# Optimization experiments

Hardware: AMD Instinct MI355X
Metric: run time of the kernel (lower is better)

## Reference

```python
import jax, jax.numpy as jnp
import numpy as np

N_ENT = 50000
N_REL = 237
DIM = 200
BATCH = 1024
N_EDGE_RAW = 400000
WALK_LEN = 3


def _build_graph():
    rng = np.random.default_rng(0)
    src = rng.integers(0, N_ENT, N_EDGE_RAW)
    dst = rng.integers(0, N_ENT, N_EDGE_RAW)
    key = np.unique(src.astype(np.int64) * N_ENT + dst.astype(np.int64))
    row = (key // N_ENT).astype(np.int64)
    col = (key % N_ENT).astype(np.int64)
    # symmetric D^{-1/2} A D^{-1/2} normalization (binary coalesced adjacency)
    deg = np.bincount(row, minlength=N_ENT).astype(np.float64)
    dinv = np.where(deg > 0, deg ** -0.5, 0.0)
    adj_val = (dinv[row] * dinv[col]).astype(np.float32)
    # random walk of length 3 from every node (torch_cluster.random_walk semantics)
    rowptr = np.concatenate([[0], np.cumsum(np.bincount(row, minlength=N_ENT))]).astype(np.int64)
    cur = np.arange(N_ENT)
    walk = [cur]
    for _ in range(WALK_LEN):
        d = rowptr[cur + 1] - rowptr[cur]
        off = np.floor(rng.random(N_ENT) * np.maximum(d, 1)).astype(np.int64)
        idx = np.minimum(rowptr[cur] + off, len(row) - 1)
        nxt = np.where(d > 0, col[idx], cur)
        walk.append(nxt)
        cur = nxt
    walk = np.stack(walk, 1)  # (N, WALK_LEN+1)
    # scatter(rw_adj, 1, walk, 1): binary rows, duplicates collapse; then D^{-1} row-normalize
    rw_key = np.unique(np.repeat(np.arange(N_ENT), WALK_LEN + 1).astype(np.int64) * N_ENT + walk.reshape(-1))
    rw_row = (rw_key // N_ENT).astype(np.int64)
    rw_col = (rw_key % N_ENT).astype(np.int64)
    rw_deg = np.bincount(rw_row, minlength=N_ENT).astype(np.float64)
    rw_val = (1.0 / np.maximum(rw_deg[rw_row], 1.0)).astype(np.float32)
    return row, col, adj_val, rw_row, rw_col, rw_val


def setup_inputs() -> dict:
    row, col, adj_val, rw_row, rw_col, rw_val = _build_graph()
    E = row.shape[0]
    key = jax.random.key(0)
    ks = jax.random.split(key, 12)
    g = 0.05
    return dict(
        entity_emb=jax.random.normal(ks[0], (N_ENT, DIM), jnp.float32) * g,
        rel_emb=jax.random.normal(ks[1], (2 * N_REL, DIM * DIM), jnp.float32) * 0.01,
        node_W1=jax.random.normal(ks[2], (2, DIM, DIM), jnp.float32) * g,
        node_b1=jnp.zeros((2, DIM), jnp.float32),
        node_W2=jax.random.normal(ks[3], (2, DIM, 1), jnp.float32) * g,
        node_b2=jnp.zeros((2, 1), jnp.float32),
        edge_W1=jax.random.normal(ks[4], (2, 2 * DIM, DIM), jnp.float32) * g,
        edge_b1=jnp.zeros((2, DIM), jnp.float32),
        edge_W2=jax.random.normal(ks[5], (2, DIM, 1), jnp.float32) * g,
        edge_b2=jnp.zeros((2, 1), jnp.float32),
        adj_row=jnp.asarray(row), adj_col=jnp.asarray(col), adj_val=jnp.asarray(adj_val),
        rw_row=jnp.asarray(rw_row), rw_col=jnp.asarray(rw_col), rw_val=jnp.asarray(rw_val),
        node_eps=jax.random.uniform(ks[6], (2, N_ENT, 1), jnp.float32),
        edge_eps=jax.random.uniform(ks[7], (2, E, 1), jnp.float32),
        sub=jax.random.randint(ks[8], (BATCH,), 0, N_ENT),
        rel=jax.random.randint(ks[9], (BATCH,), 0, 2 * N_REL),
        obj=jax.random.randint(ks[10], (BATCH,), 0, N_ENT),
        neg_tail=jax.random.randint(ks[11], (BATCH, 2), 0, N_ENT),
    )


def _spmm(row, col, val, x, n):
    # sparse COO (row, col, val) @ dense x, output (n, d)
    return jax.ops.segment_sum(val[:, None] * x[col], row, num_segments=n)


def _gate(logits, u):
    # concrete-gate noise: eps ~ U(bias, 1-bias); sigmoid((logit(eps)+logits)/0.5)
    bias = 1e-4
    eps = (2.0 * bias - 1.0) * u + (1.0 - bias)
    return jax.nn.sigmoid((jnp.log(eps) - jnp.log1p(-eps) + logits) / 0.5)


def reference(entity_emb, rel_emb, node_W1, node_b1, node_W2, node_b2,
              edge_W1, edge_b1, edge_W2, edge_b2,
              adj_row, adj_col, adj_val, rw_row, rw_col, rw_val,
              node_eps, edge_eps, sub, rel, obj, neg_tail):
    n, d = entity_emb.shape
    e0 = entity_emb
    node_masks, edge_masks = [], []
    edge_cat = jnp.concatenate([e0[adj_row], e0[adj_col]], axis=-1)  # (E, 2d)
    for i in range(2):
        h = jax.nn.relu(e0 @ node_W1[i] + node_b1[i])
        node_masks.append(_gate(h @ node_W2[i] + node_b2[i], node_eps[i]))  # (n,1)
        he = jax.nn.relu(edge_cat @ edge_W1[i] + edge_b1[i])
        edge_masks.append(_gate(he @ edge_W2[i] + edge_b2[i], edge_eps[i])[:, 0])  # (E,)
    # node-drop branch: mix self vs random-walk mean-pooled, then GCN propagate
    x_nd = e0
    for i in range(2):
        mp = _spmm(rw_row, rw_col, rw_val, x_nd, n)
        x_nd = node_masks[i] * x_nd + (1.0 - node_masks[i]) * mp
        x_nd = _spmm(adj_row, adj_col, adj_val, x_nd, n)
    # edge-drop branch: rw propagation twice; only the LAST edge mask is applied (as in source)
    x_ed = e0
    new_edge = adj_val
    for i in range(2):
        x_ed = _spmm(rw_row, rw_col, rw_val, x_ed, n)
        new_edge = adj_val * edge_masks[i]
    x_ed = _spmm(adj_row, adj_col, new_edge, x_ed, n)
    # RESCAL scoring against all entities
    lhs1 = e0[sub]                                   # (B, d)
    rel1 = rel_emb[rel].reshape(-1, d, d)            # (B, d, d)
    self_hr = jnp.einsum('bd,bde->be', lhs1, rel1)   # (B, d)
    scores = jax.nn.sigmoid(self_hr @ e0.T)          # (B, n)
    return scores, x_nd, x_ed
```

## Files before the change

### kernel.cpp

```cpp
#include <hip/hip_runtime.h>
#include <math.h>

#define DIMV 200
typedef unsigned short ushort;
typedef unsigned int uint;
typedef __attribute__((ext_vector_type(8))) __bf16  bf16x8;
typedef __attribute__((ext_vector_type(4))) float   f32x4;

static __device__ __forceinline__ int lower_bound(const int* __restrict__ a, int n, int key) {
    int lo = 0, hi = n;
    while (lo < hi) {
        int mid = (lo + hi) >> 1;
        if (a[mid] < key) lo = mid + 1; else hi = mid;
    }
    return lo;
}

static __device__ __forceinline__ float gate_fn(float u, float logit) {
    float ee = fmaf(u, -0.9998f, 0.9999f);
    float g  = (logf(ee) - log1pf(-ee) + logit) * 2.0f;
    return 1.0f / (1.0f + expf(-g));
}

static __device__ __forceinline__ ushort f2bf(float f) {
    unsigned int u = __float_as_uint(f);
    return (ushort)((u + 0x7fffu + ((u >> 16) & 1u)) >> 16);
}
static __device__ __forceinline__ float2 bfp2f(uint u) {
    float2 r;
    r.x = __uint_as_float(u << 16);
    r.y = __uint_as_float(u & 0xffff0000u);
    return r;
}
static __device__ __forceinline__ uint f2bfp(float a, float b) {
    return (uint)f2bf(a) | ((uint)f2bf(b) << 16);
}

static __device__ __forceinline__ void cvt8_store(ushort* dst, const float* src) {
    float4 a = *(const float4*)src;
    float4 b = *(const float4*)(src + 4);
    dst[0] = f2bf(a.x); dst[1] = f2bf(a.y); dst[2] = f2bf(a.z); dst[3] = f2bf(a.w);
    dst[4] = f2bf(b.x); dst[5] = f2bf(b.y); dst[6] = f2bf(b.z); dst[7] = f2bf(b.w);
}
static __device__ __forceinline__ void zero8_store(ushort* dst) {
#pragma unroll
    for (int i = 0; i < 8; i++) dst[i] = 0;
}

__global__ __launch_bounds__(256) void prep_all(
    const float* __restrict__ e0, ushort* __restrict__ e0bf,
    const float* __restrict__ w1e_src, ushort* __restrict__ W1eT,
    const float* __restrict__ w1n_src, ushort* __restrict__ W1nT,
    const int* __restrict__ adj_row, int E, int* __restrict__ rp_adj,
    const int* __restrict__ rw_row, int Erw, int* __restrict__ rp_rw,
    const float* __restrict__ rel_emb, const int* __restrict__ sub,
    const int* __restrict__ rel, ushort* __restrict__ hrbf, int N)
{
    __shared__ float lhs[DIMV];
    int bid = blockIdx.x;
    const int t = threadIdx.x;

    const int NB0 = (N * 28 + 255) >> 8;
    if (bid < NB0) {
        int idx = bid * 256 + t;
        if (idx < N * 28) {
            int n = idx / 28, c = idx % 28;
            ushort* dst = e0bf + (size_t)n * 224 + c * 8;
            if (c < 25) cvt8_store(dst, e0 + (size_t)n * 200 + c * 8);
            else        zero8_store(dst);
        }
        return;
    }
    bid -= NB0;
    if (bid < 364) {
        int idx = bid * 256 + t;
        if (idx < 416 * 224) {
            int n = idx / 224, k = idx % 224;
            float v = 0.f;
            if (k < 200) {
                if (n < 200)      v = w1e_src[k * 200 + n];
                else if (n < 400) v = w1e_src[(k + 200) * 200 + (n - 200)];
            }
            W1eT[idx] = f2bf(v);
        }
        return;
    }
    bid -= 364;
    if (bid < 364) {
        int i = bid / 182;
        int idx = (bid % 182) * 256 + t;
        if (idx < 208 * 224) {
            int n = idx / 224, k = idx % 224;
            float v = (n < 200 && k < 200) ? w1n_src[i * 40000 + k * 200 + n] : 0.f;
            W1nT[(size_t)i * 208 * 224 + idx] = f2bf(v);
        }
        return;
    }
    bid -= 364;
    const int NBr = (N + 256) >> 8;
    if (bid < NBr) {
        int r = bid * 256 + t;
        if (r <= N) rp_adj[r] = lower_bound(adj_row, E, r);
        return;
    }
    bid -= NBr;
    if (bid < NBr) {
        int r = bid * 256 + t;
        if (r <= N) rp_rw[r] = lower_bound(rw_row, Erw, r);
        return;
    }
    bid -= NBr;
    {
        const int b = bid;
        if (t < DIMV) lhs[t] = e0[(size_t)sub[b] * DIMV + t];
        __syncthreads();
        if (t >= 224) return;
        if (t < DIMV) {
            const float* R = rel_emb + (size_t)rel[b] * (DIMV * DIMV);
            float acc = 0.f;
            for (int dd = 0; dd < DIMV; dd++)
                acc = fmaf(lhs[dd], R[dd * DIMV + t], acc);
            hrbf[(size_t)b * 224 + t] = f2bf(acc);
        } else {
            hrbf[(size_t)b * 224 + t] = 0;
        }
    }
}

__global__ __launch_bounds__(256) void fused_mlp(
    const ushort* __restrict__ e0bf, const ushort* __restrict__ W1eT,
    const ushort* __restrict__ W1nT, ushort* __restrict__ Pb,
    const float* __restrict__ nb1, const float* __restrict__ nW2,
    const float* __restrict__ nb2, const float* __restrict__ neps,
    float* __restrict__ node_mask, int N, int GX)
{
    __shared__ __align__(16) ushort As[2][128 * 40];
    __shared__ __align__(16) ushort Bs[2][208 * 40];
    __shared__ float bsh[208], wsh[208];

    const int r8  = blockIdx.x & 7;
    const int rem = blockIdx.x >> 3;
    const int y   = rem & 3;
    const int q4  = rem >> 2;
    const int x   = r8 + 8 * q4;
    if (x >= GX) return;

    const int t    = threadIdx.x;
    const int lane = t & 63;
    const int w    = t >> 6;
    const int q    = lane >> 4;
    const int ln   = lane & 15;
    const int r0   = x * 128;
    const bool edge = (y < 2);
    const int  i    = y - 2;
    const ushort* Wt = edge ? (W1eT + (size_t)y * 208 * 224)
                            : (W1nT + (size_t)i * 208 * 224);

    if (!edge && t < 208) {
        bsh[t] = (t < 200) ? nb1[i * 200 + t] : 0.f;
        wsh[t] = (t < 200) ? nW2[i * 200 + t] : 0.f;
    }

    f32x4 acc[2][13];
#pragma unroll
    for (int mt = 0; mt < 2; mt++)
#pragma unroll
        for (int nt = 0; nt < 13; nt++) {
            acc[mt][nt][0] = 0.f; acc[mt][nt][1] = 0.f;
            acc[mt][nt][2] = 0.f; acc[mt][nt][3] = 0.f;
        }

    auto stageA = [&](int ks, int buf) {
#pragma unroll
        for (int it = 0; it < 2; it++) {
            int f = t + it * 256;
            int m = f >> 2, c4 = f & 3;
            int g = r0 + m;
            ushort* dst = &As[buf][m * 40 + c4 * 8];
            if (g < N) *(bf16x8*)dst = *(const bf16x8*)&e0bf[(size_t)g * 224 + ks * 32 + c4 * 8];
            else       zero8_store(dst);
        }
    };
    auto stageB = [&](int ks, int buf) {
        for (int f = t; f < 832; f += 256) {
            int n = f >> 2, c4 = f & 3;
            *(bf16x8*)&Bs[buf][n * 40 + c4 * 8] =
                *(const bf16x8*)&Wt[(size_t)n * 224 + ks * 32 + c4 * 8];
        }
    };

    stageA(0, 0); stageB(0, 0);
    __syncthreads();

    for (int ks = 0; ks < 7; ks++) {
        int cur = ks & 1;
        if (ks + 1 < 7) { stageA(ks + 1, cur ^ 1); stageB(ks + 1, cur ^ 1); }
        bf16x8 af0 = *(const bf16x8*)&As[cur][(w * 32 + ln) * 40 + q * 8];
        bf16x8 af1 = *(const bf16x8*)&As[cur][(w * 32 + 16 + ln) * 40 + q * 8];
#pragma unroll
        for (int nt = 0; nt < 13; nt++) {
            bf16x8 bf = *(const bf16x8*)&Bs[cur][(nt * 16 + ln) * 40 + q * 8];
            acc[0][nt] = __builtin_amdgcn_mfma_f32_16x16x32_bf16(af0, bf, acc[0][nt], 0, 0, 0);
            acc[1][nt] = __builtin_amdgcn_mfma_f32_16x16x32_bf16(af1, bf, acc[1][nt], 0, 0, 0);
        }
        __syncthreads();
    }

    if (edge) {
#pragma unroll
        for (int mt = 0; mt < 2; mt++) {
            int gm = r0 + w * 32 + mt * 16 + q * 4;
#pragma unroll
            for (int nt = 0; nt < 13; nt++) {
                int gn = y * 208 + nt * 16 + ln;
                if (gn < 400) {
#pragma unroll
                    for (int r = 0; r < 4; r++)
                        if (gm + r < N) Pb[(size_t)(gm + r) * 400 + gn] = f2bf(acc[mt][nt][r]);
                }
            }
        }
    } else {
        float p[2][4];
#pragma unroll
        for (int mt = 0; mt < 2; mt++)
#pragma unroll
            for (int r = 0; r < 4; r++) {
                float s = 0.f;
#pragma unroll
                for (int nt = 0; nt < 13; nt++) {
                    int n = nt * 16 + ln;
                    float h = fmaxf(acc[mt][nt][r] + bsh[n], 0.f);
                    s = fmaf(h, wsh[n], s);
                }
                p[mt][r] = s;
            }
#pragma unroll
        for (int off = 1; off < 16; off <<= 1)
#pragma unroll
            for (int mt = 0; mt < 2; mt++)
#pragma unroll
                for (int r = 0; r < 4; r++)
                    p[mt][r] += __shfl_xor(p[mt][r], off);

        if (ln == 0) {
            float b2v = nb2[i];
            const float* epsi = neps + (size_t)i * N;
            float* outi = node_mask + (size_t)i * N;
#pragma unroll
            for (int mt = 0; mt < 2; mt++)
#pragma unroll
                for (int r = 0; r < 4; r++) {
                    int g = r0 + w * 32 + mt * 16 + q * 4 + r;
                    if (g < N) outi[g] = gate_fn(epsi[g], p[mt][r] + b2v);
                }
        }
    }
}

static __device__ __forceinline__ void spmm_bb_body(
    const uint* __restrict__ x, int xld, const int* __restrict__ rowptr,
    const int* __restrict__ col, const float* __restrict__ val,
    uint* __restrict__ out, int N, int vb, int t)
{
    const int w = t >> 6, lane = t & 63;
    const int r = vb * 4 + w;
    if (lane >= 50 || r >= N) return;
    const int off = 2 * lane;
    const int lo = rowptr[r], hi = rowptr[r + 1];
    float a0 = 0.f, a1 = 0.f, a2 = 0.f, a3 = 0.f;
    for (int e = lo; e < hi; e += 4) {
        int n = hi - e;
        int c0 = col[e];
        int c1 = n > 1 ? col[e + 1] : c0;
        int c2 = n > 2 ? col[e + 2] : c0;
        int c3 = n > 3 ? col[e + 3] : c0;
        float v0 = val[e];
        float v1 = n > 1 ? val[e + 1] : 0.f;
        float v2 = n > 2 ? val[e + 2] : 0.f;
        float v3 = n > 3 ? val[e + 3] : 0.f;
        uint2 u0 = *(const uint2*)&x[(size_t)c0 * xld + off];
        uint2 u1 = *(const uint2*)&x[(size_t)c1 * xld + off];
        uint2 u2 = *(const uint2*)&x[(size_t)c2 * xld + off];
        uint2 u3 = *(const uint2*)&x[(size_t)c3 * xld + off];
        float2 p;
        p = bfp2f(u0.x); a0 = fmaf(v0, p.x, a0); a1 = fmaf(v0, p.y, a1);
        p = bfp2f(u0.y); a2 = fmaf(v0, p.x, a2); a3 = fmaf(v0, p.y, a3);
        p = bfp2f(u1.x); a0 = fmaf(v1, p.x, a0); a1 = fmaf(v1, p.y, a1);
        p = bfp2f(u1.y); a2 = fmaf(v1, p.x, a2); a3 = fmaf(v1, p.y, a3);
        p = bfp2f(u2.x); a0 = fmaf(v2, p.x, a0); a1 = fmaf(v2, p.y, a1);
        p = bfp2f(u2.y); a2 = fmaf(v2, p.x, a2); a3 = fmaf(v2, p.y, a3);
        p = bfp2f(u3.x); a0 = fmaf(v3, p.x, a0); a1 = fmaf(v3, p.y, a1);
        p = bfp2f(u3.y); a2 = fmaf(v3, p.x, a2); a3 = fmaf(v3, p.y, a3);
    }
    *(uint2*)&out[(size_t)r * 100 + off] = make_uint2(f2bfp(a0, a1), f2bfp(a2, a3));
}

static __device__ __forceinline__ void dual_body(
    const uint* __restrict__ xA, const uint* __restrict__ xB,
    const int* __restrict__ rowptr, const int* __restrict__ col,
    const float* __restrict__ val, const float* __restrict__ emask,
    float* __restrict__ outA, uint* __restrict__ outB, int N, int vb, int t)
{
    const int w = t >> 6, lane = t & 63;
    const int r = vb * 4 + w;
    if (lane >= 50 || r >= N) return;
    const int off = 2 * lane;
    const int lo = rowptr[r], hi = rowptr[r + 1];
    float sA0=0.f,sA1=0.f,sA2=0.f,sA3=0.f;
    float sB0=0.f,sB1=0.f,sB2=0.f,sB3=0.f;
    for (int e = lo; e < hi; e += 4) {
        int n = hi - e;
        int c0 = col[e];
        int c1 = n > 1 ? col[e + 1] : c0;
        int c2 = n > 2 ? col[e + 2] : c0;
        int c3 = n > 3 ? col[e + 3] : c0;
        float v0 = val[e];
        float v1 = n > 1 ? val[e + 1] : 0.f;
        float v2 = n > 2 ? val[e + 2] : 0.f;
        float v3 = n > 3 ? val[e + 3] : 0.f;
        float m0 = v0 * emask[e];
        float m1 = n > 1 ? v1 * emask[e + 1] : 0.f;
        float m2 = n > 2 ? v2 * emask[e + 2] : 0.f;
        float m3 = n > 3 ? v3 * emask[e + 3] : 0.f;
        size_t o0 = (size_t)c0 * 100 + off, o1 = (size_t)c1 * 100 + off;
        size_t o2 = (size_t)c2 * 100 + off, o3 = (size_t)c3 * 100 + off;
        uint2 ua0 = *(const uint2*)&xA[o0], ua1 = *(const uint2*)&xA[o1];
        uint2 ua2 = *(const uint2*)&xA[o2], ua3 = *(const uint2*)&xA[o3];
        uint2 ub0 = *(const uint2*)&xB[o0], ub1 = *(const uint2*)&xB[o1];
        uint2 ub2 = *(const uint2*)&xB[o2], ub3 = *(const uint2*)&xB[o3];
        float2 p;
        p = bfp2f(ua0.x); sA0 = fmaf(m0, p.x, sA0); sA1 = fmaf(m0, p.y, sA1);
        p = bfp2f(ua0.y); sA2 = fmaf(m0, p.x, sA2); sA3 = fmaf(m0, p.y, sA3);
        p = bfp2f(ua1.x); sA0 = fmaf(m1, p.x, sA0); sA1 = fmaf(m1, p.y, sA1);
        p = bfp2f(ua1.y); sA2 = fmaf(m1, p.x, sA2); sA3 = fmaf(m1, p.y, sA3);
        p = bfp2f(ua2.x); sA0 = fmaf(m2, p.x, sA0); sA1 = fmaf(m2, p.y, sA1);
        p = bfp2f(ua2.y); sA2 = fmaf(m2, p.x, sA2); sA3 = fmaf(m2, p.y, sA3);
        p = bfp2f(ua3.x); sA0 = fmaf(m3, p.x, sA0); sA1 = fmaf(m3, p.y, sA1);
        p = bfp2f(ua3.y); sA2 = fmaf(m3, p.x, sA2); sA3 = fmaf(m3, p.y, sA3);
        p = bfp2f(ub0.x); sB0 = fmaf(v0, p.x, sB0); sB1 = fmaf(v0, p.y, sB1);
        p = bfp2f(ub0.y); sB2 = fmaf(v0, p.x, sB2); sB3 = fmaf(v0, p.y, sB3);
        p = bfp2f(ub1.x); sB0 = fmaf(v1, p.x, sB0); sB1 = fmaf(v1, p.y, sB1);
        p = bfp2f(ub1.y); sB2 = fmaf(v1, p.x, sB2); sB3 = fmaf(v1, p.y, sB3);
        p = bfp2f(ub2.x); sB0 = fmaf(v2, p.x, sB0); sB1 = fmaf(v2, p.y, sB1);
        p = bfp2f(ub2.y); sB2 = fmaf(v2, p.x, sB2); sB3 = fmaf(v2, p.y, sB3);
        p = bfp2f(ub3.x); sB0 = fmaf(v3, p.x, sB0); sB1 = fmaf(v3, p.y, sB1);
        p = bfp2f(ub3.y); sB2 = fmaf(v3, p.x, sB2); sB3 = fmaf(v3, p.y, sB3);
    }
    float4 oA; oA.x = sA0; oA.y = sA1; oA.z = sA2; oA.w = sA3;
    *(float4*)&outA[(size_t)r * 200 + 2 * off] = oA;
    *(uint2*)&outB[(size_t)r * 100 + off] = make_uint2(f2bfp(sB0, sB1), f2bfp(sB2, sB3));
}

static __device__ __forceinline__ void rwcomb_body(
    const uint* __restrict__ x, const int* __restrict__ rowptr,
    const int* __restrict__ col, const float* __restrict__ val,
    const float* __restrict__ mask, uint* __restrict__ out, int N, int vb, int t)
{
    const int w = t >> 6, lane = t & 63;
    const int r = vb * 4 + w;
    if (lane >= 50 || r >= N) return;
    const int off = 2 * lane;
    const int lo = rowptr[r], hi = rowptr[r + 1];
    float a0 = 0.f, a1 = 0.f, a2 = 0.f, a3 = 0.f;
    for (int e = lo; e < hi; e += 4) {
        int n = hi - e;
        int c0 = col[e];
        int c1 = n > 1 ? col[e + 1] : c0;
        int c2 = n > 2 ? col[e + 2] : c0;
        int c3 = n > 3 ? col[e + 3] : c0;
        float v0 = val[e];
        float v1 = n > 1 ? val[e + 1] : 0.f;
        float v2 = n > 2 ? val[e + 2] : 0.f;
        float v3 = n > 3 ? val[e + 3] : 0.f;
        uint2 u0 = *(const uint2*)&x[(size_t)c0 * 100 + off];
        uint2 u1 = *(const uint2*)&x[(size_t)c1 * 100 + off];
        uint2 u2 = *(const uint2*)&x[(size_t)c2 * 100 + off];
        uint2 u3 = *(const uint2*)&x[(size_t)c3 * 100 + off];
        float2 p;
        p = bfp2f(u0.x); a0 = fmaf(v0, p.x, a0); a1 = fmaf(v0, p.y, a1);
        p = bfp2f(u0.y); a2 = fmaf(v0, p.x, a2); a3 = fmaf(v0, p.y, a3);
        p = bfp2f(u1.x); a0 = fmaf(v1, p.x, a0); a1 = fmaf(v1, p.y, a1);
        p = bfp2f(u1.y); a2 = fmaf(v1, p.x, a2); a3 = fmaf(v1, p.y, a3);
        p = bfp2f(u2.x); a0 = fmaf(v2, p.x, a0); a1 = fmaf(v2, p.y, a1);
        p = bfp2f(u2.y); a2 = fmaf(v2, p.x, a2); a3 = fmaf(v2, p.y, a3);
        p = bfp2f(u3.x); a0 = fmaf(v3, p.x, a0); a1 = fmaf(v3, p.y, a1);
        p = bfp2f(u3.y); a2 = fmaf(v3, p.x, a2); a3 = fmaf(v3, p.y, a3);
    }
    const float m = mask[r];
    uint2 xs = *(const uint2*)&x[(size_t)r * 100 + off];
    float2 xa = bfp2f(xs.x), xb = bfp2f(xs.y);
    *(uint2*)&out[(size_t)r * 100 + off] = make_uint2(
        f2bfp(fmaf(m, xa.x - a0, a0), fmaf(m, xa.y - a1, a1)),
        f2bfp(fmaf(m, xb.x - a2, a2), fmaf(m, xb.y - a3, a3)));
}

static __device__ __forceinline__ void bf32_body(
    const uint* __restrict__ x, const int* __restrict__ rowptr,
    const int* __restrict__ col, const float* __restrict__ val,
    float* __restrict__ out, int N, int vb, int t)
{
    const int w = t >> 6, lane = t & 63;
    const int r = vb * 4 + w;
    if (lane >= 50 || r >= N) return;
    const int off = 2 * lane;
    const int lo = rowptr[r], hi = rowptr[r + 1];
    float a0 = 0.f, a1 = 0.f, a2 = 0.f, a3 = 0.f;
    for (int e = lo; e < hi; e += 8) {
        int n = hi - e;
        int c0 = col[e];
        int c1 = n > 1 ? col[e + 1] : c0;
        int c2 = n > 2 ? col[e + 2] : c0;
        int c3 = n > 3 ? col[e + 3] : c0;
        int c4 = n > 4 ? col[e + 4] : c0;
        int c5 = n > 5 ? col[e + 5] : c0;
        int c6 = n > 6 ? col[e + 6] : c0;
        int c7 = n > 7 ? col[e + 7] : c0;
        float v0 = val[e];
        float v1 = n > 1 ? val[e + 1] : 0.f;
        float v2 = n > 2 ? val[e + 2] : 0.f;
        float v3 = n > 3 ? val[e + 3] : 0.f;
        float v4 = n > 4 ? val[e + 4] : 0.f;
        float v5 = n > 5 ? val[e + 5] : 0.f;
        float v6 = n > 6 ? val[e + 6] : 0.f;
        float v7 = n > 7 ? val[e + 7] : 0.f;
        uint2 u0 = *(const uint2*)&x[(size_t)c0 * 100 + off];
        uint2 u1 = *(const uint2*)&x[(size_t)c1 * 100 + off];
        uint2 u2 = *(const uint2*)&x[(size_t)c2 * 100 + off];
        uint2 u3 = *(const uint2*)&x[(size_t)c3 * 100 + off];
        uint2 u4 = *(const uint2*)&x[(size_t)c4 * 100 + off];
        uint2 u5 = *(const uint2*)&x[(size_t)c5 * 100 + off];
        uint2 u6 = *(const uint2*)&x[(size_t)c6 * 100 + off];
        uint2 u7 = *(const uint2*)&x[(size_t)c7 * 100 + off];
        float2 p;
        p = bfp2f(u0.x); a0 = fmaf(v0, p.x, a0); a1 = fmaf(v0, p.y, a1);
        p = bfp2f(u0.y); a2 = fmaf(v0, p.x, a2); a3 = fmaf(v0, p.y, a3);
        p = bfp2f(u1.x); a0 = fmaf(v1, p.x, a0); a1 = fmaf(v1, p.y, a1);
        p = bfp2f(u1.y); a2 = fmaf(v1, p.x, a2); a3 = fmaf(v1, p.y, a3);
        p = bfp2f(u2.x); a0 = fmaf(v2, p.x, a0); a1 = fmaf(v2, p.y, a1);
        p = bfp2f(u2.y); a2 = fmaf(v2, p.x, a2); a3 = fmaf(v2, p.y, a3);
        p = bfp2f(u3.x); a0 = fmaf(v3, p.x, a0); a1 = fmaf(v3, p.y, a1);
        p = bfp2f(u3.y); a2 = fmaf(v3, p.x, a2); a3 = fmaf(v3, p.y, a3);
        p = bfp2f(u4.x); a0 = fmaf(v4, p.x, a0); a1 = fmaf(v4, p.y, a1);
        p = bfp2f(u4.y); a2 = fmaf(v4, p.x, a2); a3 = fmaf(v4, p.y, a3);
        p = bfp2f(u5.x); a0 = fmaf(v5, p.x, a0); a1 = fmaf(v5, p.y, a1);
        p = bfp2f(u5.y); a2 = fmaf(v5, p.x, a2); a3 = fmaf(v5, p.y, a3);
        p = bfp2f(u6.x); a0 = fmaf(v6, p.x, a0); a1 = fmaf(v6, p.y, a1);
        p = bfp2f(u6.y); a2 = fmaf(v6, p.x, a2); a3 = fmaf(v6, p.y, a3);
        p = bfp2f(u7.x); a0 = fmaf(v7, p.x, a0); a1 = fmaf(v7, p.y, a1);
        p = bfp2f(u7.y); a2 = fmaf(v7, p.x, a2); a3 = fmaf(v7, p.y, a3);
    }
    float4 o; o.x = a0; o.y = a1; o.z = a2; o.w = a3;
    *(float4*)&out[(size_t)r * 200 + 2 * off] = o;
}

static __device__ __forceinline__ void egate_body(
    int vb, int t, const uint* __restrict__ P4, const int* __restrict__ rp_adj,
    const int* __restrict__ adj_col, const float* __restrict__ eps,
    float* __restrict__ edge_mask, int N,
    const float* __restrict__ eb1, const float* __restrict__ eW2, float b2v)
{
    const int w = t >> 6, lane = t & 63;
    const int r = vb * 4 + w;
    if (r >= N) return;
    const bool act = lane < 50;
    const int off = act ? 2 * lane : 0;
    float4 bb, ww;
    if (act) { bb = *(const float4*)&eb1[4 * lane]; ww = *(const float4*)&eW2[4 * lane]; }
    else     { bb.x = bb.y = bb.z = bb.w = 0.f; ww.x = ww.y = ww.z = ww.w = 0.f; }

    uint2 pr = *(const uint2*)&P4[(size_t)r * 200 + off];
    float2 pA = bfp2f(pr.x), pB = bfp2f(pr.y);
    const float h0 = pA.x + bb.x, h1 = pA.y + bb.y;
    const float h2 = pB.x + bb.z, h3 = pB.y + bb.w;

    const int lo = rp_adj[r], hi = rp_adj[r + 1];
    for (int e = lo; e < hi; e += 4) {
        int n = hi - e;
        int c0 = adj_col[e];
        int c1 = n > 1 ? adj_col[e + 1] : c0;
        int c2 = n > 2 ? adj_col[e + 2] : c0;
        int c3 = n > 3 ? adj_col[e + 3] : c0;
        uint2 q0 = *(const uint2*)&P4[(size_t)c0 * 200 + 100 + off];
        uint2 q1 = *(const uint2*)&P4[(size_t)c1 * 200 + 100 + off];
        uint2 q2 = *(const uint2*)&P4[(size_t)c2 * 200 + 100 + off];
        uint2 q3 = *(const uint2*)&P4[(size_t)c3 * 200 + 100 + off];
        float2 qa, qb;
        qa = bfp2f(q0.x); qb = bfp2f(q0.y);
        float s0 = fmaxf(h0 + qa.x, 0.f) * ww.x + fmaxf(h1 + qa.y, 0.f) * ww.y
                 + fmaxf(h2 + qb.x, 0.f) * ww.z + fmaxf(h3 + qb.y, 0.f) * ww.w;
        qa = bfp2f(q1.x); qb = bfp2f(q1.y);
        float s1 = fmaxf(h0 + qa.x, 0.f) * ww.x + fmaxf(h1 + qa.y, 0.f) * ww.y
                 + fmaxf(h2 + qb.x, 0.f) * ww.z + fmaxf(h3 + qb.y, 0.f) * ww.w;
        qa = bfp2f(q2.x); qb = bfp2f(q2.y);
        float s2 = fmaxf(h0 + qa.x, 0.f) * ww.x + fmaxf(h1 + qa.y, 0.f) * ww.y
                 + fmaxf(h2 + qb.x, 0.f) * ww.z + fmaxf(h3 + qb.y, 0.f) * ww.w;
        qa = bfp2f(q3.x); qb = bfp2f(q3.y);
        float s3 = fmaxf(h0 + qa.x, 0.f) * ww.x + fmaxf(h1 + qa.y, 0.f) * ww.y
                 + fmaxf(h2 + qb.x, 0.f) * ww.z + fmaxf(h3 + qb.y, 0.f) * ww.w;
#pragma unroll
        for (int o = 32; o; o >>= 1) {
            s0 += __shfl_xor(s0, o); s1 += __shfl_xor(s1, o);
            s2 += __shfl_xor(s2, o); s3 += __shfl_xor(s3, o);
        }
        if (lane < 4 && e + lane < hi) {
            float sv = (lane == 0) ? s0 : (lane == 1) ? s1 : (lane == 2) ? s2 : s3;
            edge_mask[e + lane] = gate_fn(eps[e + lane], sv + b2v);
        }
    }
}

__global__ __launch_bounds__(256) void k3_rw1_egate(
    const uint* __restrict__ e0u, const int* __restrict__ rp_rw,
    const int* __restrict__ rw_col, const float* __restrict__ rw_val,
    uint* __restrict__ Tb, const uint* __restrict__ P4,
    const int* __restrict__ rp_adj, const int* __restrict__ adj_col,
    const float* __restrict__ eb1, const float* __restrict__ eW2,
    const float* __restrict__ eb2, const float* __restrict__ eeps,
    float* __restrict__ edge_mask, int N, int NB_CH)
{
    int bid = blockIdx.x;
    const int t = threadIdx.x;
    if (bid < NB_CH) { spmm_bb_body(e0u, 112, rp_rw, rw_col, rw_val, Tb, N, bid, t); return; }
    egate_body(bid - NB_CH, t, P4, rp_adj, adj_col, eeps, edge_mask, N, eb1, eW2, eb2[0]);
}

__global__ __launch_bounds__(256) void k4_rw2_combine(
    const uint* __restrict__ Tb, const int* __restrict__ rp_rw,
    const int* __restrict__ rw_col, const float* __restrict__ rw_val,
    uint* __restrict__ T2b, const float* __restrict__ e0,
    const float* __restrict__ mask, uint* __restrict__ xndb, int N, int NB_CH)
{
    int bid = blockIdx.x;
    const int t = threadIdx.x;
    if (bid < NB_CH) { spmm_bb_body(Tb, 100, rp_rw, rw_col, rw_val, T2b, N, bid, t); return; }
    int idx = (bid - NB_CH) * 256 + t;
    if (idx >= N * 100) return;
    float m = mask[idx / 100];
    float2 a = ((const float2*)e0)[idx];
    float2 b = bfp2f(Tb[idx]);
    xndb[idx] = f2bfp(fmaf(m, a.x - b.x, b.x), fmaf(m, a.y - b.y, b.y));
}

__global__ __launch_bounds__(256) void k5_dual(
    const uint* __restrict__ xA, const uint* __restrict__ xB,
    const int* __restrict__ rowptr, const int* __restrict__ col,
    const float* __restrict__ val, const float* __restrict__ emask,
    float* __restrict__ outA, uint* __restrict__ outB, int N)
{
    dual_body(xA, xB, rowptr, col, val, emask, outA, outB, N, blockIdx.x, threadIdx.x);
}

__global__ __launch_bounds__(256) void k6_rwcomb(
    const uint* __restrict__ x, const int* __restrict__ rowptr,
    const int* __restrict__ col, const float* __restrict__ val,
    const float* __restrict__ mask, uint* __restrict__ out, int N)
{
    rwcomb_body(x, rowptr, col, val, mask, out, N, blockIdx.x, threadIdx.x);
}

__global__ __launch_bounds__(256) void k7_bf32(
    const uint* __restrict__ x, const int* __restrict__ rowptr,
    const int* __restrict__ col, const float* __restrict__ val,
    float* __restrict__ out, int N)
{
    bf32_body(x, rowptr, col, val, out, N, blockIdx.x, threadIdx.x);
}

__global__ __launch_bounds__(256) void scores_mfma(
    const ushort* __restrict__ hrbf, const ushort* __restrict__ e0bf,
    float* __restrict__ scores, int Nent, int GX)
{
    __shared__ __align__(16) ushort Bs[2][192 * 40];

    const int r8  = blockIdx.x & 7;
    const int rem = blockIdx.x >> 3;
    const int y   = rem & 7;
    const int q8  = rem >> 3;
    const int x   = r8 + 8 * q8;
    if (x >= GX) return;

    const int t    = threadIdx.x;
    const int lane = t & 63;
    const int w    = t >> 6;
    const int q    = lane >> 4;
    const int ln   = lane & 15;
    const int n0   = x * 192;
    const int b0   = y * 128;
    const int arow = b0 + w * 32 + ln;

    auto stageB = [&](int ks, int buf) {
        for (int f = t; f < 768; f += 256) {
            int n = f >> 2, c4 = f & 3;
            int gn = n0 + n;
            ushort* dst = &Bs[buf][n * 40 + c4 * 8];
            if (gn < Nent) *(bf16x8*)dst = *(const bf16x8*)&e0bf[(size_t)gn * 224 + ks * 32 + c4 * 8];
            else           zero8_store(dst);
        }
    };
    stageB(0, 0);

    f32x4 acc[2][12];
#pragma unroll
    for (int mt = 0; mt < 2; mt++)
#pragma unroll
        for (int nt = 0; nt < 12; nt++) {
            acc[mt][nt][0] = 0.f; acc[mt][nt][1] = 0.f;
            acc[mt][nt][2] = 0.f; acc[mt][nt][3] = 0.f;
        }

    bf16x8 a0 = *(const bf16x8*)&hrbf[(size_t)arow * 224 + q * 8];
    bf16x8 a1 = *(const bf16x8*)&hrbf[(size_t)(arow + 16) * 224 + q * 8];
    __syncthreads();

    for (int ks = 0; ks < 7; ks++) {
        int cur = ks & 1;
        bf16x8 a0n = a0, a1n = a1;
        if (ks + 1 < 7) {
            stageB(ks + 1, cur ^ 1);
            a0n = *(const bf16x8*)&hrbf[(size_t)arow * 224 + (ks + 1) * 32 + q * 8];
            a1n = *(const bf16x8*)&hrbf[(size_t)(arow + 16) * 224 + (ks + 1) * 32 + q * 8];
        }
#pragma unroll
        for (int nt = 0; nt < 12; nt++) {
            bf16x8 bf = *(const bf16x8*)&Bs[cur][(nt * 16 + ln) * 40 + q * 8];
            acc[0][nt] = __builtin_amdgcn_mfma_f32_16x16x32_bf16(a0, bf, acc[0][nt], 0, 0, 0);
            acc[1][nt] = __builtin_amdgcn_mfma_f32_16x16x32_bf16(a1, bf, acc[1][nt], 0, 0, 0);
        }
        __syncthreads();
        a0 = a0n; a1 = a1n;
    }

#pragma unroll
    for (int mt = 0; mt < 2; mt++) {
        int b = b0 + w * 32 + mt * 16 + q * 4;
#pragma unroll
        for (int nt = 0; nt < 12; nt++) {
            int n = n0 + nt * 16 + ln;
            if (n < Nent) {
#pragma unroll
                for (int r = 0; r < 4; r++)
                    scores[(size_t)(b + r) * Nent + n] = 1.f / (1.f + __expf(-acc[mt][nt][r]));
            }
        }
    }
}

extern "C" void kernel_launch(void* const* d_in, const int* in_sizes, int n_in,
                              void* d_out, int out_size, void* d_ws, size_t ws_size,
                              hipStream_t stream)
{
    const float* e0       = (const float*)d_in[0];
    const float* rel_emb  = (const float*)d_in[1];
    const float* node_W1  = (const float*)d_in[2];
    const float* node_b1  = (const float*)d_in[3];
    const float* node_W2  = (const float*)d_in[4];
    const float* node_b2  = (const float*)d_in[5];
    const float* edge_W1  = (const float*)d_in[6];
    const float* edge_b1  = (const float*)d_in[7];
    const float* edge_W2  = (const float*)d_in[8];
    const float* edge_b2  = (const float*)d_in[9];
    const int*   adj_row  = (const int*)d_in[10];
    const int*   adj_col  = (const int*)d_in[11];
    const float* adj_val  = (const float*)d_in[12];
    const int*   rw_row   = (const int*)d_in[13];
    const int*   rw_col   = (const int*)d_in[14];
    const float* rw_val   = (const float*)d_in[15];
    const float* node_eps = (const float*)d_in[16];
    const float* edge_eps = (const float*)d_in[17];
    const int*   sub      = (const int*)d_in[18];
    const int*   rel      = (const int*)d_in[19];

    const int E   = in_sizes[10];
    const int Erw = in_sizes[13];
    const int N   = in_sizes[0] / DIMV;
    const int B   = in_sizes[18];

    ushort* W1eT = (ushort*)d_ws;
    ushort* W1nT = W1eT + 416 * 224;
    ushort* e0bf = W1nT + 2 * 208 * 224;
    ushort* hrbf = e0bf + (size_t)N * 224;
    float*  fb   = (float*)(hrbf + (size_t)B * 224);
    float*  node_mask = fb;
    float*  edge_mask = node_mask + 2 * (size_t)N;
    int*    rp_adj = (int*)(edge_mask + E);
    int*    rp_rw  = rp_adj + (N + 1);

    float* out    = (float*)d_out;
    float* scores = out;
    float* x_nd   = out + (size_t)B * N;
    float* x_ed   = x_nd + (size_t)N * DIMV;
    uint*   Tb   = (uint*)scores;
    uint*   T2b  = Tb   + (size_t)N * 100;
    uint*   xndb = T2b  + (size_t)N * 100;
    uint*   Tnb  = xndb + (size_t)N * 100;
    uint*   Pb   = Tnb  + (size_t)N * 100;

    const int NB_CH = (N + 3) / 4;
    const int CB    = (N * 100 + 255) / 256;
    const int NB0   = (N * 28 + 255) / 256;
    const int NBr   = (N + 256) / 256;
    const int prep_blocks = NB0 + 364 + 364 + NBr + NBr + B;
    const int GXg = (N + 127) / 128;
    const int GXs = (N + 191) / 192;

    prep_all<<<prep_blocks, 256, 0, stream>>>(
        e0, e0bf, edge_W1 + 400 * 200, W1eT, node_W1, W1nT,
        adj_row, E, rp_adj, rw_row, Erw, rp_rw,
        rel_emb, sub, rel, hrbf, N);

    fused_mlp<<<32 * ((GXg + 7) / 8), 256, 0, stream>>>(
        e0bf, W1eT, W1nT, (ushort*)Pb,
        node_b1, node_W2, node_b2, node_eps, node_mask, N, GXg);

    k3_rw1_egate<<<2 * NB_CH, 256, 0, stream>>>(
        (const uint*)e0bf, rp_rw, rw_col, rw_val, Tb, Pb, rp_adj, adj_col,
        edge_b1 + 200, edge_W2 + 200, edge_b2 + 1, edge_eps + (size_t)E,
        edge_mask, N, NB_CH);

    k4_rw2_combine<<<NB_CH + CB, 256, 0, stream>>>(
        Tb, rp_rw, rw_col, rw_val, T2b, e0, node_mask, xndb, N, NB_CH);

    k5_dual<<<NB_CH, 256, 0, stream>>>(
        T2b, xndb, rp_adj, adj_col, adj_val, edge_mask, x_ed, Tnb, N);

    k6_rwcomb<<<NB_CH, 256, 0, stream>>>(
        Tnb, rp_rw, rw_col, rw_val, node_mask + N, T2b, N);

    k7_bf32<<<NB_CH, 256, 0, stream>>>(T2b, rp_adj, adj_col, adj_val, x_nd, N);

    scores_mfma<<<64 * ((GXs + 7) / 8), 256, 0, stream>>>(
        hrbf, e0bf, scores, N, GXs);
}
```

Measured before the change: 831.0 us.

## Interleave scores GEMM slices into the sparse propagation kernels

Splits the RESCAL scoring GEMM into eight 128-row batch slices. It launches them as extra blocks inside the rw/adj SpMM kernels (k3–k6), leaving the rest for a final scores kernel, so the dense MFMA work overlaps the latency-bound sparse gathers. The scratch buffers that alias the scores output are reordered so each slice is written only after the scratch data beneath it is no longer read. The slice schedule is enabled only for the N=50000, B=1024 shape. The block-index swizzle the old scores kernel used for L2 locality is dropped, and both workloads now compete for memory bandwidth.

```diff
diff --git a/kernel.cpp b/kernel.cpp
--- a/kernel.cpp
+++ b/kernel.cpp
@@ -256,6 +256,80 @@
                 }
         }
     }
+}
+
+static __device__ void scores_body(
+    const ushort* __restrict__ hrbf, const ushort* __restrict__ e0bf,
+    float* __restrict__ scores, int Nent, int x, int b0, int t)
+{
+    __shared__ __align__(16) ushort Bs[2][192 * 40];
+
+    const int lane = t & 63;
+    const int w    = t >> 6;
+    const int q    = lane >> 4;
+    const int ln   = lane & 15;
+    const int n0   = x * 192;
+    const int arow = b0 + w * 32 + ln;
+
+    auto stageB = [&](int ks, int buf) {
+        for (int f = t; f < 768; f += 256) {
+            int n = f >> 2, c4 = f & 3;
+            int gn = n0 + n;
+            ushort* dst = &Bs[buf][n * 40 + c4 * 8];
+            if (gn < Nent) *(bf16x8*)dst = *(const bf16x8*)&e0bf[(size_t)gn * 224 + ks * 32 + c4 * 8];
+            else           zero8_store(dst);
+        }
+    };
+    stageB(0, 0);
+
+    f32x4 acc[2][12];
+#pragma unroll
+    for (int mt = 0; mt < 2; mt++)
+#pragma unroll
+        for (int nt = 0; nt < 12; nt++) {
+            acc[mt][nt][0] = 0.f; acc[mt][nt][1] = 0.f;
+            acc[mt][nt][2] = 0.f; acc[mt][nt][3] = 0.f;
+        }
+
+    bf16x8 a0 = *(const bf16x8*)&hrbf[(size_t)arow * 224 + q * 8];
+    bf16x8 a1 = *(const bf16x8*)&hrbf[(size_t)(arow + 16) * 224 + q * 8];
+    __syncthreads();
+
+    for (int ks = 0; ks < 7; ks++) {
+        int cur = ks & 1;
+        bf16x8 a0n = a0, a1n = a1;
+        if (ks + 1 < 7) {
+            stageB(ks + 1, cur ^ 1);
+            a0n = *(const bf16x8*)&hrbf[(size_t)arow * 224 + (ks + 1) * 32 + q * 8];
+            a1n = *(const bf16x8*)&hrbf[(size_t)(arow + 16) * 224 + (ks + 1) * 32 + q * 8];
+        }
+#pragma unroll
+        for (int nt = 0; nt < 12; nt++) {
+            bf16x8 bf = *(const bf16x8*)&Bs[cur][(nt * 16 + ln) * 40 + q * 8];
+            acc[0][nt] = __builtin_amdgcn_mfma_f32_16x16x32_bf16(a0, bf, acc[0][nt], 0, 0, 0);
+            acc[1][nt] = __builtin_amdgcn_mfma_f32_16x16x32_bf16(a1, bf, acc[1][nt], 0, 0, 0);
+        }
+        __syncthreads();
+        a0 = a0n; a1 = a1n;
+    }
+
+#pragma unroll
+    for (int mt = 0; mt < 2; mt++) {
+        int b = b0 + w * 32 + mt * 16 + q * 4;
+#pragma unroll
+        for (int nt = 0; nt < 12; nt++) {
+            int n = n0 + nt * 16 + ln;
+            if (n < Nent) {
+#pragma unroll
+                for (int r = 0; r < 4; r++)
+                    scores[(size_t)(b + r) * Nent + n] = 1.f / (1.f + __expf(-acc[mt][nt][r]));
+            }
+        }
+    }
+}
+
+static __device__ __forceinline__ int slice_y(int sl, int ns, int ya, int yb) {
+    return (ns == 8) ? sl : (sl == 0 ? ya : yb);
 }
 
 static __device__ __forceinline__ void spmm_bb_body(
@@ -517,10 +591,18 @@
     const int* __restrict__ rp_adj, const int* __restrict__ adj_col,
     const float* __restrict__ eb1, const float* __restrict__ eW2,
     const float* __restrict__ eb2, const float* __restrict__ eeps,
-    float* __restrict__ edge_mask, int N, int NB_CH)
+    float* __restrict__ edge_mask, int N, int NB_CH,
+    const ushort* __restrict__ hrbf, const ushort* __restrict__ e0bf,
+    float* __restrict__ scores, int GXs, int ns, int ya, int yb)
 {
     int bid = blockIdx.x;
     const int t = threadIdx.x;
+    if (bid < ns * GXs) {
+        int sl = bid / GXs;
+        scores_body(hrbf, e0bf, scores, N, bid % GXs, slice_y(sl, ns, ya, yb) * 128, t);
+        return;
+    }
+    bid -= ns * GXs;
     if (bid < NB_CH) { spmm_bb_body(e0u, 112, rp_rw, rw_col, rw_val, Tb, N, bid, t); return; }
     egate_body(bid - NB_CH, t, P4, rp_adj, adj_col, eeps, edge_mask, N, eb1, eW2, eb2[0]);
 }
@@ -529,10 +611,18 @@
     const uint* __restrict__ Tb, const int* __restrict__ rp_rw,
     const int* __restrict__ rw_col, const float* __restrict__ rw_val,
     uint* __restrict__ T2b, const float* __restrict__ e0,
-    const float* __restrict__ mask, uint* __restrict__ xndb, int N, int NB_CH)
+    const float* __restrict__ mask, uint* __restrict__ xndb, int N, int NB_CH,
+    const ushort* __restrict__ hrbf, const ushort* __restrict__ e0bf,
+    float* __restrict__ scores, int GXs, int ns, int ya, int yb)
 {
     int bid = blockIdx.x;
     const int t = threadIdx.x;
+    if (bid < ns * GXs) {
+        int sl = bid / GXs;
+        scores_body(hrbf, e0bf, scores, N, bid % GXs, slice_y(sl, ns, ya, yb) * 128, t);
+        return;
+    }
+    bid -= ns * GXs;
     if (bid < NB_CH) { spmm_bb_body(Tb, 100, rp_rw, rw_col, rw_val, T2b, N, bid, t); return; }
     int idx = (bid - NB_CH) * 256 + t;
     if (idx >= N * 100) return;
@@ -546,17 +636,35 @@
     const uint* __restrict__ xA, const uint* __restrict__ xB,
     const int* __restrict__ rowptr, const int* __restrict__ col,
     const float* __restrict__ val, const float* __restrict__ emask,
-    float* __restrict__ outA, uint* __restrict__ outB, int N)
-{
-    dual_body(xA, xB, rowptr, col, val, emask, outA, outB, N, blockIdx.x, threadIdx.x);
+    float* __restrict__ outA, uint* __restrict__ outB, int N,
+    const ushort* __restrict__ hrbf, const ushort* __restrict__ e0bf,
+    float* __restrict__ scores, int GXs, int ns, int ya, int yb)
+{
+    int bid = blockIdx.x;
+    const int t = threadIdx.x;
+    if (bid < ns * GXs) {
+        int sl = bid / GXs;
+        scores_body(hrbf, e0bf, scores, N, bid % GXs, slice_y(sl, ns, ya, yb) * 128, t);
+        return;
+    }
+    dual_body(xA, xB, rowptr, col, val, emask, outA, outB, N, bid - ns * GXs, t);
 }
 
 __global__ __launch_bounds__(256) void k6_rwcomb(
     const uint* __restrict__ x, const int* __restrict__ rowptr,
     const int* __restrict__ col, const float* __restrict__ val,
-    const float* __restrict__ mask, uint* __restrict__ out, int N)
-{
-    rwcomb_body(x, rowptr, col, val, mask, out, N, blockIdx.x, threadIdx.x);
+    const float* __restrict__ mask, uint* __restrict__ out, int N,
+    const ushort* __restrict__ hrbf, const ushort* __restrict__ e0bf,
+    float* __restrict__ scores, int GXs, int ns, int ya, int yb)
+{
+    int bid = blockIdx.x;
+    const int t = threadIdx.x;
+    if (bid < ns * GXs) {
+        int sl = bid / GXs;
+        scores_body(hrbf, e0bf, scores, N, bid % GXs, slice_y(sl, ns, ya, yb) * 128, t);
+        return;
+    }
+    rwcomb_body(x, rowptr, col, val, mask, out, N, bid - ns * GXs, t);
 }
 
 __global__ __launch_bounds__(256) void k7_bf32(
@@ -567,83 +675,15 @@
     bf32_body(x, rowptr, col, val, out, N, blockIdx.x, threadIdx.x);
 }
 
-__global__ __launch_bounds__(256) void scores_mfma(
+__global__ __launch_bounds__(256) void k8_scores(
     const ushort* __restrict__ hrbf, const ushort* __restrict__ e0bf,
-    float* __restrict__ scores, int Nent, int GX)
-{
-    __shared__ __align__(16) ushort Bs[2][192 * 40];
-
-    const int r8  = blockIdx.x & 7;
-    const int rem = blockIdx.x >> 3;
-    const int y   = rem & 7;
-    const int q8  = rem >> 3;
-    const int x   = r8 + 8 * q8;
-    if (x >= GX) return;
-
-    const int t    = threadIdx.x;
-    const int lane = t & 63;
-    const int w    = t >> 6;
-    const int q    = lane >> 4;
-    const int ln   = lane & 15;
-    const int n0   = x * 192;
-    const int b0   = y * 128;
-    const int arow = b0 + w * 32 + ln;
-
-    auto stageB = [&](int ks, int buf) {
-        for (int f = t; f < 768; f += 256) {
-            int n = f >> 2, c4 = f & 3;
-            int gn = n0 + n;
-            ushort* dst = &Bs[buf][n * 40 + c4 * 8];
-            if (gn < Nent) *(bf16x8*)dst = *(const bf16x8*)&e0bf[(size_t)gn * 224 + ks * 32 + c4 * 8];
-            else           zero8_store(dst);
-        }
-    };
-    stageB(0, 0);
-
-    f32x4 acc[2][12];
-#pragma unroll
-    for (int mt = 0; mt < 2; mt++)
-#pragma unroll
-        for (int nt = 0; nt < 12; nt++) {
-            acc[mt][nt][0] = 0.f; acc[mt][nt][1] = 0.f;
-            acc[mt][nt][2] = 0.f; acc[mt][nt][3] = 0.f;
-        }
-
-    bf16x8 a0 = *(const bf16x8*)&hrbf[(size_t)arow * 224 + q * 8];
-    bf16x8 a1 = *(const bf16x8*)&hrbf[(size_t)(arow + 16) * 224 + q * 8];
-    __syncthreads();
-
-    for (int ks = 0; ks < 7; ks++) {
-        int cur = ks & 1;
-        bf16x8 a0n = a0, a1n = a1;
-        if (ks + 1 < 7) {
-            stageB(ks + 1, cur ^ 1);
-            a0n = *(const bf16x8*)&hrbf[(size_t)arow * 224 + (ks + 1) * 32 + q * 8];
-            a1n = *(const bf16x8*)&hrbf[(size_t)(arow + 16) * 224 + (ks + 1) * 32 + q * 8];
-        }
-#pragma unroll
-        for (int nt = 0; nt < 12; nt++) {
-            bf16x8 bf = *(const bf16x8*)&Bs[cur][(nt * 16 + ln) * 40 + q * 8];
-            acc[0][nt] = __builtin_amdgcn_mfma_f32_16x16x32_bf16(a0, bf, acc[0][nt], 0, 0, 0);
-            acc[1][nt] = __builtin_amdgcn_mfma_f32_16x16x32_bf16(a1, bf, acc[1][nt], 0, 0, 0);
-        }
-        __syncthreads();
-        a0 = a0n; a1 = a1n;
-    }
-
-#pragma unroll
-    for (int mt = 0; mt < 2; mt++) {
-        int b = b0 + w * 32 + mt * 16 + q * 4;
-#pragma unroll
-        for (int nt = 0; nt < 12; nt++) {
-            int n = n0 + nt * 16 + ln;
-            if (n < Nent) {
-#pragma unroll
-                for (int r = 0; r < 4; r++)
-                    scores[(size_t)(b + r) * Nent + n] = 1.f / (1.f + __expf(-acc[mt][nt][r]));
-            }
-        }
-    }
+    float* __restrict__ scores, int Nent, int GXs, int ns, int ya, int yb)
+{
+    int bid = blockIdx.x;
+    if (bid >= ns * GXs) return;
+    int sl = bid / GXs;
+    scores_body(hrbf, e0bf, scores, Nent, bid % GXs,
+                slice_y(sl, ns, ya, yb) * 128, threadIdx.x);
 }
 
 extern "C" void kernel_launch(void* const* d_in, const int* in_sizes, int n_in,
@@ -690,11 +730,11 @@
     float* scores = out;
     float* x_nd   = out + (size_t)B * N;
     float* x_ed   = x_nd + (size_t)N * DIMV;
-    uint*   Tb   = (uint*)scores;
-    uint*   T2b  = Tb   + (size_t)N * 100;
-    uint*   xndb = T2b  + (size_t)N * 100;
+    uint*   Pb   = (uint*)scores;
+    uint*   Tb   = Pb   + (size_t)N * 200;
+    uint*   xndb = Tb   + (size_t)N * 100;
     uint*   Tnb  = xndb + (size_t)N * 100;
-    uint*   Pb   = Tnb  + (size_t)N * 100;
+    uint*   T2b  = Tnb  + (size_t)N * 100;
 
     const int NB_CH = (N + 3) / 4;
     const int CB    = (N * 100 + 255) / 256;
@@ -704,6 +744,13 @@
     const int GXg = (N + 127) / 128;
     const int GXs = (N + 191) / 192;
 
+    const bool ovl = (N == 50000 && B == 1024);
+    const int ns3 = ovl ? 1 : 0, y3a = 5, y3b = 5;
+    const int ns4 = ovl ? 2 : 0, y4a = 0, y4b = 6;
+    const int ns5 = ovl ? 2 : 0, y5a = 1, y5b = 7;
+    const int ns6 = ovl ? 1 : 0, y6a = 2, y6b = 2;
+    const int ns8 = ovl ? 2 : 8, y8a = 3, y8b = 4;
+
     prep_all<<<prep_blocks, 256, 0, stream>>>(
         e0, e0bf, edge_W1 + 400 * 200, W1eT, node_W1, W1nT,
         adj_row, E, rp_adj, rw_row, Erw, rp_rw,
@@ -713,22 +760,25 @@
         e0bf, W1eT, W1nT, (ushort*)Pb,
         node_b1, node_W2, node_b2, node_eps, node_mask, N, GXg);
 
-    k3_rw1_egate<<<2 * NB_CH, 256, 0, stream>>>(
+    k3_rw1_egate<<<ns3 * GXs + 2 * NB_CH, 256, 0, stream>>>(
         (const uint*)e0bf, rp_rw, rw_col, rw_val, Tb, Pb, rp_adj, adj_col,
         edge_b1 + 200, edge_W2 + 200, edge_b2 + 1, edge_eps + (size_t)E,
-        edge_mask, N, NB_CH);
-
-    k4_rw2_combine<<<NB_CH + CB, 256, 0, stream>>>(
-        Tb, rp_rw, rw_col, rw_val, T2b, e0, node_mask, xndb, N, NB_CH);
-
-    k5_dual<<<NB_CH, 256, 0, stream>>>(
-        T2b, xndb, rp_adj, adj_col, adj_val, edge_mask, x_ed, Tnb, N);
-
-    k6_rwcomb<<<NB_CH, 256, 0, stream>>>(
-        Tnb, rp_rw, rw_col, rw_val, node_mask + N, T2b, N);
+        edge_mask, N, NB_CH, hrbf, e0bf, scores, GXs, ns3, y3a, y3b);
+
+    k4_rw2_combine<<<ns4 * GXs + NB_CH + CB, 256, 0, stream>>>(
+        Tb, rp_rw, rw_col, rw_val, T2b, e0, node_mask, xndb, N, NB_CH,
+        hrbf, e0bf, scores, GXs, ns4, y4a, y4b);
+
+    k5_dual<<<ns5 * GXs + NB_CH, 256, 0, stream>>>(
+        T2b, xndb, rp_adj, adj_col, adj_val, edge_mask, x_ed, Tnb, N,
+        hrbf, e0bf, scores, GXs, ns5, y5a, y5b);
+
+    k6_rwcomb<<<ns6 * GXs + NB_CH, 256, 0, stream>>>(
+        Tnb, rp_rw, rw_col, rw_val, node_mask + N, T2b, N,
+        hrbf, e0bf, scores, GXs, ns6, y6a, y6b);
 
     k7_bf32<<<NB_CH, 256, 0, stream>>>(T2b, rp_adj, adj_col, adj_val, x_nd, N);
 
-    scores_mfma<<<64 * ((GXs + 7) / 8), 256, 0, stream>>>(
-        hrbf, e0bf, scores, N, GXs);
-}
+    k8_scores<<<ns8 * GXs, 256, 0, stream>>>(
+        hrbf, e0bf, scores, N, GXs, ns8, y8a, y8b);
+}
```

New measurement: 1.496 ms. +80.1%, slower.
